# Optimization experiments

Measured on AMD Instinct MI355X. Metric: run time of the kernel, lower is better.

## Reference

```python
import jax, jax.numpy as jnp
import numpy as np

B, T, C = 2, 2048, 1024
HS, DS = 8, 32      # short heads, short qk dim
HL, DL = 8, 128     # long heads, long qk dim
HD = 64             # value/output head dim = n_embd // n_head
WIN_S, WIN_L = 256, 1024
NEG = jnp.finfo(jnp.float32).min


def _window_mask(t, window):
    # additive mask: disallow future (i<j) and tokens older than the window
    i = jnp.arange(t)[:, None]
    j = jnp.arange(t)[None, :]
    bad = (i - j < 0) | (i - j >= window)
    return bad.astype(jnp.float32) * NEG  # [T,T]


def _attn(x, Wqk, Wv, n_h, d_qk, d_v, window):
    b, t, _ = x.shape
    qk = x @ Wqk                                      # [B,T,2*n_h*d_qk]
    q, k = jnp.split(qk, 2, axis=-1)
    q = q.reshape(b, t, n_h, d_qk).transpose(0, 2, 1, 3)  # [B,H,T,dqk]
    k = k.reshape(b, t, n_h, d_qk).transpose(0, 2, 1, 3)
    v = (x @ Wv).reshape(b, t, n_h, d_v).transpose(0, 2, 1, 3)  # [B,H,T,dv]
    scale = 1.0 / jnp.sqrt(jnp.float32(d_qk))
    scores = jnp.einsum('bhqd,bhkd->bhqk', q, k) * scale
    scores = scores + _window_mask(t, window)
    p = jax.nn.softmax(scores, axis=-1)
    return jnp.einsum('bhqk,bhkd->bhqd', p, v)        # [B,H,T,dv]


def setup_inputs() -> dict:
    key = jax.random.key(0)
    ks = jax.random.split(key, 6)
    s = 0.02
    return {
        'x': jax.random.normal(ks[0], (B, T, C), dtype=jnp.float32),
        'Wqk_short': jax.random.normal(ks[1], (C, 2 * HS * DS), dtype=jnp.float32) * s,
        'Wv_short': jax.random.normal(ks[2], (C, HS * HD), dtype=jnp.float32) * s,
        'Wqk_long': jax.random.normal(ks[3], (C, 2 * HL * DL), dtype=jnp.float32) * s,
        'Wv_long': jax.random.normal(ks[4], (C, HL * HD), dtype=jnp.float32) * s,
        'Wproj': jax.random.normal(ks[5], (C, C), dtype=jnp.float32) * s,
    }


def reference(x, Wqk_short, Wv_short, Wqk_long, Wv_long, Wproj):
    b, t, c = x.shape
    y_short = _attn(x, Wqk_short, Wv_short, HS, DS, HD, WIN_S)  # [B,HS,T,HD]
    y_long = _attn(x, Wqk_long, Wv_long, HL, DL, HD, WIN_L)     # [B,HL,T,HD]
    y = jnp.concatenate([y_short, y_long], axis=1)              # [B,H,T,HD]
    y = y.transpose(0, 2, 1, 3).reshape(b, t, c)
    return y @ Wproj
```

## Files before the change

kernel.cpp:

```cpp
#include <hip/hip_runtime.h>
#include <math.h>

#define B_    2
#define T_    2048
#define C_    1024
#define HS_   8
#define DS_   32
#define HL_   8
#define DL_   128
#define HD_   64
#define WINS_ 256
#define WINL_ 1024
#define NALL_ 3584

typedef __bf16 bf16x8 __attribute__((ext_vector_type(8)));
typedef float floatx4 __attribute__((ext_vector_type(4)));

__device__ __forceinline__ ushort f2bf(float f) {
    union { float f; unsigned u; } v; v.f = f;
    unsigned r = v.u + 0x7fff + ((v.u >> 16) & 1);
    return (ushort)(r >> 16);
}

__device__ __forceinline__ void gload_lds16(const void* g, void* l) {
    __builtin_amdgcn_global_load_lds(
        (const __attribute__((address_space(1))) void*)g,
        (__attribute__((address_space(3))) void*)l, 16, 0, 0);
}

__global__ __launch_bounds__(256) void prep(
    const float* __restrict__ x, ushort* __restrict__ x16,
    const float* __restrict__ Wqk_s, const float* __restrict__ Wv_s,
    const float* __restrict__ Wqk_l, const float* __restrict__ Wv_l,
    const float* __restrict__ Wproj, ushort* __restrict__ WallT,
    ushort* __restrict__ WprojT) {
    __shared__ float t[32][33];
    int bid = blockIdx.x;
    if (bid < 4096) {
        const int i = bid * 256 + threadIdx.x;
        float4 v = ((const float4*)x)[i];
        ushort4 o;
        o.x = f2bf(v.x); o.y = f2bf(v.y); o.z = f2bf(v.z); o.w = f2bf(v.w);
        ((ushort4*)x16)[i] = o;
        return;
    }
    bid -= 4096;
    const float* W; ushort* WT; int N, rowoff;
    if (bid < 512)       { W = Wqk_s; WT = WallT;  N = 512;  rowoff = 0; }
    else if (bid < 1024) { bid -= 512;  W = Wv_s;  WT = WallT;  N = 512;  rowoff = 512; }
    else if (bid < 3072) { bid -= 1024; W = Wqk_l; WT = WallT;  N = 2048; rowoff = 1024; }
    else if (bid < 3584) { bid -= 3072; W = Wv_l;  WT = WallT;  N = 512;  rowoff = 3072; }
    else                 { bid -= 3584; W = Wproj; WT = WprojT; N = 1024; rowoff = 0; }
    const int nt = N / 32;
    const int n0 = (bid % nt) * 32;
    const int k0 = (bid / nt) * 32;
    const int tx = threadIdx.x & 31;
    const int ty = threadIdx.x >> 5;
#pragma unroll
    for (int i = 0; i < 4; ++i)
        t[ty + 8 * i][tx] = W[(size_t)(k0 + ty + 8 * i) * N + n0 + tx];
    __syncthreads();
#pragma unroll
    for (int i = 0; i < 4; ++i)
        WT[(size_t)(rowoff + n0 + ty + 8 * i) * 1024 + k0 + tx] =
            f2bf(t[tx][ty + 8 * i]);
}

template <typename OT>
__global__ __launch_bounds__(256) void gemm_bf16(const ushort* __restrict__ A,
                                                 const ushort* __restrict__ BT,
                                                 OT* __restrict__ Cm,
                                                 int M, int N, int K) {
    __shared__ ushort As[128 * 32];
    __shared__ ushort Bs[128 * 32];
    const int tid = threadIdx.x;
    const int m0 = blockIdx.y * 128;
    const int n0 = blockIdx.x * 128;
    const int wave = tid >> 6;
    const int lane = tid & 63;
    const int wm = (wave >> 1) * 64;
    const int wn = (wave & 1) * 64;
    const int l15 = lane & 15;
    const int quad = lane >> 4;

    const int srow = tid >> 2;
    const int sc = (tid & 3) * 8;

    floatx4 acc[4][4] = {};

    const ushort* Ap0 = A + (size_t)(m0 + srow) * K + sc;
    const ushort* Ap1 = A + (size_t)(m0 + srow + 64) * K + sc;
    const ushort* Bp0 = BT + (size_t)(n0 + srow) * K + sc;
    const ushort* Bp1 = BT + (size_t)(n0 + srow + 64) * K + sc;

    ushort* AsB0 = &As[wave * 512];
    ushort* AsB1 = &As[wave * 512 + 2048];
    ushort* BsB0 = &Bs[wave * 512];
    ushort* BsB1 = &Bs[wave * 512 + 2048];

    for (int kt = 0; kt < K; kt += 32) {
        __syncthreads();
        gload_lds16(Ap0 + kt, AsB0);
        gload_lds16(Ap1 + kt, AsB1);
        gload_lds16(Bp0 + kt, BsB0);
        gload_lds16(Bp1 + kt, BsB1);
        __syncthreads();

        bf16x8 af[4], bfr[4];
#pragma unroll
        for (int i = 0; i < 4; ++i)
            af[i] = *(const bf16x8*)&As[(wm + i * 16 + l15) * 32 + quad * 8];
#pragma unroll
        for (int j = 0; j < 4; ++j)
            bfr[j] = *(const bf16x8*)&Bs[(wn + j * 16 + l15) * 32 + quad * 8];
#pragma unroll
        for (int i = 0; i < 4; ++i)
#pragma unroll
            for (int j = 0; j < 4; ++j)
                acc[i][j] = __builtin_amdgcn_mfma_f32_16x16x32_bf16(
                    af[i], bfr[j], acc[i][j], 0, 0, 0);
    }

#pragma unroll
    for (int i = 0; i < 4; ++i)
#pragma unroll
        for (int j = 0; j < 4; ++j)
#pragma unroll
            for (int r = 0; r < 4; ++r) {
                const size_t idx = (size_t)(m0 + wm + i * 16 + quad * 4 + r) * N +
                                   n0 + wn + j * 16 + l15;
                if constexpr (sizeof(OT) == 2)
                    Cm[idx] = f2bf(acc[i][j][r]);
                else
                    Cm[idx] = acc[i][j][r];
            }
}

__global__ __launch_bounds__(256) void vtrans(const ushort* __restrict__ act,
                                              ushort* __restrict__ vt) {
    __shared__ ushort tile[64][72];
    const int t0 = blockIdx.x * 64;
    const int gh = blockIdx.y;
    const int b = blockIdx.z;
    const int col = (gh < 8) ? (512 + gh * 64) : (3072 + (gh - 8) * 64);
    const ushort* src = act + (size_t)(b * T_ + t0) * NALL_ + col;
    {
        const int tr = threadIdx.x >> 2;
        const int ch = threadIdx.x & 3;
        *(int4*)&tile[tr][ch * 8] =
            *(const int4*)(src + (size_t)tr * NALL_ + ch * 8);
        *(int4*)&tile[tr][(ch + 4) * 8] =
            *(const int4*)(src + (size_t)tr * NALL_ + (ch + 4) * 8);
    }
    __syncthreads();
    const int d = threadIdx.x >> 2;
    const int ts = (threadIdx.x & 3) * 16;
    ushort tmp[16];
#pragma unroll
    for (int i = 0; i < 16; ++i) tmp[i] = tile[ts + i][d];
    ushort* dst = vt + ((size_t)(b * 16 + gh) * HD_ + d) * T_ + t0 + ts;
    *(int4*)dst = *(int4*)tmp;
    *(int4*)(dst + 8) = *(int4*)(tmp + 8);
}

template <int D, int WIN, bool SPLIT>
__device__ __forceinline__ void attn_dev(
    const ushort* __restrict__ act, const ushort* __restrict__ vt,
    ushort* __restrict__ y, float* __restrict__ po, float* __restrict__ pm,
    float* __restrict__ pl, float scale, int qoff, int koff, int head_off,
    int h, int gh, int b, int t0, int zs, ushort* lds) {
    constexpr int STR = D + 8;
    constexpr int PSTR = 72;
    constexpr int NKS = D / 32;
    constexpr int QCH = D / 8;
    constexpr int NKLD = (64 * QCH) / 256;

    ushort* Ks = lds;
    ushort* VTs = Ks + 64 * STR;
    ushort* Ps = VTs + 64 * PSTR;

    const int tid = threadIdx.x;
    const int wave = tid >> 6;
    const int lane = tid & 63;
    const int l15 = lane & 15;
    const int quad = lane >> 4;
    const int qmin = t0 + wave * 16;

    int k0s = t0 - WIN + 1;
    if (k0s < 0) k0s = 0;
    k0s &= ~63;

    int ks_begin = k0s, ks_last = t0;
    if (SPLIT) {
        const int nt = ((t0 - k0s) >> 6) + 1;
        const int ntlo = (nt + 1) >> 1;
        if (zs == 0) {
            ks_last = k0s + (ntlo - 1) * 64;
        } else {
            if (ntlo >= nt) {
#pragma unroll
                for (int r = 0; r < 4; ++r) {
                    const int t = qmin + quad * 4 + r;
                    const size_t ridx =
                        (((size_t)(zs * 2 + b) * 8 + h) * T_ + t);
                    if (l15 == 0) { pm[ridx] = -1e30f; pl[ridx] = 0.f; }
#pragma unroll
                    for (int j = 0; j < 4; ++j)
                        po[ridx * 64 + j * 16 + l15] = 0.f;
                }
                return;
            }
            ks_begin = k0s + ntlo * 64;
        }
    }

    const ushort* qbase = act + (size_t)(b * T_ + t0) * NALL_ + qoff + h * D;
    const ushort* kbase = act + (size_t)(b * T_) * NALL_ + koff + h * D;
    const ushort* vtb = vt + (size_t)((b * 16 + gh) * HD_) * T_;

    int krow[NKLD], kch[NKLD];
#pragma unroll
    for (int i = 0; i < NKLD; ++i) {
        const int idx = tid + 256 * i;
        krow[i] = idx / QCH;
        kch[i] = idx % QCH;
    }
    const int vd0 = tid >> 3, vc0 = (tid & 7) * 8;
    const int vd1 = (tid + 256) >> 3, vc1 = ((tid + 256) & 7) * 8;

    int4 kreg[NKLD], vreg0, vreg1;
#pragma unroll
    for (int i = 0; i < NKLD; ++i)
        kreg[i] =
            *(const int4*)(kbase + (size_t)(ks_begin + krow[i]) * NALL_ + kch[i] * 8);
    vreg0 = *(const int4*)(vtb + (size_t)vd0 * T_ + ks_begin + vc0);
    vreg1 = *(const int4*)(vtb + (size_t)vd1 * T_ + ks_begin + vc1);

    for (int idx = tid; idx < 64 * QCH; idx += 256) {
        const int row = idx / QCH;
        const int ch = idx % QCH;
        *(int4*)&Ks[row * STR + ch * 8] =
            *(const int4*)(qbase + (size_t)row * NALL_ + ch * 8);
    }
    __syncthreads();
    bf16x8 qa[NKS];
#pragma unroll
    for (int ks = 0; ks < NKS; ++ks)
        qa[ks] = *(const bf16x8*)&Ks[(wave * 16 + l15) * STR + ks * 32 + quad * 8];

    float m_i[4], l_i[4];
    floatx4 o_acc[4] = {};
#pragma unroll
    for (int r = 0; r < 4; ++r) { m_i[r] = -1e30f; l_i[r] = 0.f; }

    for (int k0 = ks_begin; k0 <= ks_last; k0 += 64) {
        __syncthreads();
#pragma unroll
        for (int i = 0; i < NKLD; ++i)
            *(int4*)&Ks[krow[i] * STR + kch[i] * 8] = kreg[i];
        *(int4*)&VTs[vd0 * PSTR + vc0] = vreg0;
        *(int4*)&VTs[vd1 * PSTR + vc1] = vreg1;
        __syncthreads();
        if (k0 + 64 <= ks_last) {
#pragma unroll
            for (int i = 0; i < NKLD; ++i)
                kreg[i] = *(const int4*)(kbase +
                                         (size_t)(k0 + 64 + krow[i]) * NALL_ +
                                         kch[i] * 8);
            vreg0 = *(const int4*)(vtb + (size_t)vd0 * T_ + k0 + 64 + vc0);
            vreg1 = *(const int4*)(vtb + (size_t)vd1 * T_ + k0 + 64 + vc1);
        }

        floatx4 s[4] = {};
#pragma unroll
        for (int ks = 0; ks < NKS; ++ks) {
#pragma unroll
            for (int j = 0; j < 4; ++j) {
                const bf16x8 bb =
                    *(const bf16x8*)&Ks[(j * 16 + l15) * STR + ks * 32 + quad * 8];
                s[j] = __builtin_amdgcn_mfma_f32_16x16x32_bf16(qa[ks], bb, s[j],
                                                               0, 0, 0);
            }
        }

        const bool full = (k0 + 63 <= qmin) && ((qmin + 15) - k0 <= WIN - 1);
        if (full) {
#pragma unroll
            for (int j = 0; j < 4; ++j)
#pragma unroll
                for (int r = 0; r < 4; ++r) s[j][r] *= scale;
        } else {
#pragma unroll
            for (int j = 0; j < 4; ++j) {
                const int kj = k0 + j * 16 + l15;
#pragma unroll
                for (int r = 0; r < 4; ++r) {
                    const int rel = (qmin + quad * 4 + r) - kj;
                    s[j][r] = (rel < 0 || rel >= WIN) ? -1e30f : s[j][r] * scale;
                }
            }
        }

#pragma unroll
        for (int r = 0; r < 4; ++r) {
            float rm = fmaxf(fmaxf(s[0][r], s[1][r]), fmaxf(s[2][r], s[3][r]));
            rm = fmaxf(rm, __shfl_xor(rm, 1, 64));
            rm = fmaxf(rm, __shfl_xor(rm, 2, 64));
            rm = fmaxf(rm, __shfl_xor(rm, 4, 64));
            rm = fmaxf(rm, __shfl_xor(rm, 8, 64));
            const float mn = fmaxf(m_i[r], rm);
            const float a = __expf(m_i[r] - mn);
            m_i[r] = mn;
            float sum = 0.f;
#pragma unroll
            for (int j = 0; j < 4; ++j) {
                const float e = __expf(s[j][r] - mn);
                sum += e;
                Ps[(wave * 16 + quad * 4 + r) * PSTR + j * 16 + l15] = f2bf(e);
            }
            sum += __shfl_xor(sum, 1, 64);
            sum += __shfl_xor(sum, 2, 64);
            sum += __shfl_xor(sum, 4, 64);
            sum += __shfl_xor(sum, 8, 64);
            l_i[r] = l_i[r] * a + sum;
#pragma unroll
            for (int j = 0; j < 4; ++j) o_acc[j][r] *= a;
        }

#pragma unroll
        for (int kks = 0; kks < 2; ++kks) {
            const bf16x8 pa =
                *(const bf16x8*)&Ps[(wave * 16 + l15) * PSTR + kks * 32 + quad * 8];
#pragma unroll
            for (int j = 0; j < 4; ++j) {
                const bf16x8 vb =
                    *(const bf16x8*)&VTs[(j * 16 + l15) * PSTR + kks * 32 + quad * 8];
                o_acc[j] = __builtin_amdgcn_mfma_f32_16x16x32_bf16(pa, vb, o_acc[j],
                                                                   0, 0, 0);
            }
        }
    }

    if (SPLIT) {
#pragma unroll
        for (int r = 0; r < 4; ++r) {
            const int t = qmin + quad * 4 + r;
            const size_t ridx = (((size_t)(zs * 2 + b) * 8 + h) * T_ + t);
            if (l15 == 0) { pm[ridx] = m_i[r]; pl[ridx] = l_i[r]; }
#pragma unroll
            for (int j = 0; j < 4; ++j)
                po[ridx * 64 + j * 16 + l15] = o_acc[j][r];
        }
    } else {
#pragma unroll
        for (int r = 0; r < 4; ++r) {
            const float inv = 1.f / l_i[r];
            ushort* yrow = y + (size_t)(b * T_ + qmin + quad * 4 + r) * C_ +
                           head_off + h * HD_;
#pragma unroll
            for (int j = 0; j < 4; ++j)
                yrow[j * 16 + l15] = f2bf(o_acc[j][r] * inv);
        }
    }
}

__global__ __launch_bounds__(256, 4) void attn_sched(
    const ushort* __restrict__ act, const ushort* __restrict__ vt,
    ushort* __restrict__ y, float* __restrict__ po, float* __restrict__ pm,
    float* __restrict__ pl) {
    extern __shared__ ushort smem[];
    int x = blockIdx.x;
    if (x < 1024) {
        const int zs = x & 1;
        const int b = (x >> 1) & 1;
        const int h = (x >> 2) & 7;
        const int t0 = (31 - (x >> 5)) * 64;
        attn_dev<DL_, WINL_, true>(act, vt, y, po, pm, pl,
                                   0.08838834764831843f, 1024, 2048, 512, h,
                                   8 + h, b, t0, zs, smem);
    } else {
        x -= 1024;
        const int b = x & 1;
        const int h = (x >> 1) & 7;
        const int t0 = (31 - (x >> 4)) * 64;
        attn_dev<DS_, WINS_, false>(act, vt, y, po, pm, pl,
                                    0.17677669529663687f, 0, 256, 0, h, h, b,
                                    t0, 0, smem);
    }
}

__global__ __launch_bounds__(256) void combine(const float* __restrict__ po,
                                               const float* __restrict__ pm,
                                               const float* __restrict__ pl,
                                               ushort* __restrict__ y) {
    const int gid = blockIdx.x * 256 + threadIdx.x;
    const int row = gid >> 4;
    const int cg = (gid & 15) * 4;
    const int b = row >> 14;
    const int h = (row >> 11) & 7;
    const int t = row & 2047;

    const float m0 = pm[row], m1 = pm[32768 + row];
    const float l0 = pl[row], l1 = pl[32768 + row];
    const float4 o0 = *(const float4*)&po[(size_t)row * 64 + cg];
    const float4 o1 = *(const float4*)&po[(size_t)32768 * 64 + (size_t)row * 64 + cg];

    const float m = fmaxf(m0, m1);
    const float e0 = __expf(m0 - m);
    const float e1 = __expf(m1 - m);
    const float inv = 1.f / (l0 * e0 + l1 * e1);

    ushort4 r;
    r.x = f2bf((o0.x * e0 + o1.x * e1) * inv);
    r.y = f2bf((o0.y * e0 + o1.y * e1) * inv);
    r.z = f2bf((o0.z * e0 + o1.z * e1) * inv);
    r.w = f2bf((o0.w * e0 + o1.w * e1) * inv);
    *(ushort4*)&y[(size_t)(b * T_ + t) * C_ + 512 + h * 64 + cg] = r;
}

extern "C" void kernel_launch(void* const* d_in, const int* in_sizes, int n_in,
                              void* d_out, int out_size, void* d_ws,
                              size_t ws_size, hipStream_t stream) {
    const float* x         = (const float*)d_in[0];
    const float* Wqk_short = (const float*)d_in[1];
    const float* Wv_short  = (const float*)d_in[2];
    const float* Wqk_long  = (const float*)d_in[3];
    const float* Wv_long   = (const float*)d_in[4];
    const float* Wproj     = (const float*)d_in[5];
    float* out = (float*)d_out;

    const int M = B_ * T_;

    ushort* x16    = (ushort*)d_ws;
    ushort* WallT  = x16 + (size_t)M * C_;
    ushort* WprojT = WallT + (size_t)NALL_ * C_;
    ushort* yb16   = WprojT + (size_t)C_ * C_;
    ushort* act    = yb16 + (size_t)M * C_;
    ushort* vt     = act + (size_t)M * NALL_;
    float*  po     = (float*)(vt + (size_t)32 * HD_ * T_);
    float*  pm     = po + (size_t)2 * 32768 * 64;
    float*  pl     = pm + (size_t)2 * 32768;

    dim3 blk(256);
    prep<<<dim3(8704), blk, 0, stream>>>(x, x16, Wqk_short, Wv_short, Wqk_long,
                                         Wv_long, Wproj, WallT, WprojT);

    gemm_bf16<ushort><<<dim3(NALL_ / 128, M / 128), blk, 0, stream>>>(
        x16, WallT, act, M, NALL_, C_);

    vtrans<<<dim3(T_ / 64, 16, B_), blk, 0, stream>>>(act, vt);

    const int attn_lds = (64 * (DL_ + 8) + 64 * 72 * 2) * 2;
    attn_sched<<<dim3(1536), blk, attn_lds, stream>>>(act, vt, yb16, po, pm, pl);

    combine<<<dim3(2048), blk, 0, stream>>>(po, pm, pl, yb16);

    gemm_bf16<float><<<dim3(C_ / 128, M / 128), blk, 0, stream>>>(
        yb16, WprojT, out, M, C_, C_);
}
```

Baseline: 231.8 us.

## Split long-window attention four ways, store bf16 partials, use 64-row output GEMM tiles

The long-head attention KV range is now split into four partitions instead of two, giving 2048 long blocks plus the short blocks. This spreads work more evenly across CUs. Partial outputs are stored as bf16 instead of fp32 to cut the extra partial traffic, and the combine kernel now merges four partials. The projection GEMM uses 64-row M tiles so more blocks fill the GPU. Costs are more partial reads and writes, more precision loss in the partial sums, and empty partitions for short query ranges.

```diff
diff --git a/kernel.cpp b/kernel.cpp
--- a/kernel.cpp
+++ b/kernel.cpp
@@ -20,6 +20,10 @@
     union { float f; unsigned u; } v; v.f = f;
     unsigned r = v.u + 0x7fff + ((v.u >> 16) & 1);
     return (ushort)(r >> 16);
+}
+__device__ __forceinline__ float bf2f(ushort u) {
+    union { unsigned u; float f; } v; v.u = ((unsigned)u) << 16;
+    return v.f;
 }
 
 __device__ __forceinline__ void gload_lds16(const void* g, void* l) {
@@ -66,19 +70,20 @@
             f2bf(t[tx][ty + 8 * i]);
 }
 
-template <typename OT>
+template <int BM, typename OT>
 __global__ __launch_bounds__(256) void gemm_bf16(const ushort* __restrict__ A,
                                                  const ushort* __restrict__ BT,
                                                  OT* __restrict__ Cm,
                                                  int M, int N, int K) {
-    __shared__ ushort As[128 * 32];
+    __shared__ ushort As[BM * 32];
     __shared__ ushort Bs[128 * 32];
+    constexpr int NI = BM / 32;
     const int tid = threadIdx.x;
-    const int m0 = blockIdx.y * 128;
+    const int m0 = blockIdx.y * BM;
     const int n0 = blockIdx.x * 128;
     const int wave = tid >> 6;
     const int lane = tid & 63;
-    const int wm = (wave >> 1) * 64;
+    const int wm = (wave >> 1) * (BM / 2);
     const int wn = (wave & 1) * 64;
     const int l15 = lane & 15;
     const int quad = lane >> 4;
@@ -86,35 +91,35 @@
     const int srow = tid >> 2;
     const int sc = (tid & 3) * 8;
 
-    floatx4 acc[4][4] = {};
+    floatx4 acc[NI][4] = {};
 
     const ushort* Ap0 = A + (size_t)(m0 + srow) * K + sc;
-    const ushort* Ap1 = A + (size_t)(m0 + srow + 64) * K + sc;
+    const ushort* Ap1 = A + (size_t)(m0 + (srow & 63) + 64) * K + sc;
     const ushort* Bp0 = BT + (size_t)(n0 + srow) * K + sc;
     const ushort* Bp1 = BT + (size_t)(n0 + srow + 64) * K + sc;
 
     ushort* AsB0 = &As[wave * 512];
-    ushort* AsB1 = &As[wave * 512 + 2048];
+    ushort* AsB1 = &As[(wave * 512 + 2048) % (BM * 32)];
     ushort* BsB0 = &Bs[wave * 512];
     ushort* BsB1 = &Bs[wave * 512 + 2048];
 
     for (int kt = 0; kt < K; kt += 32) {
         __syncthreads();
         gload_lds16(Ap0 + kt, AsB0);
-        gload_lds16(Ap1 + kt, AsB1);
+        if constexpr (BM == 128) gload_lds16(Ap1 + kt, AsB1);
         gload_lds16(Bp0 + kt, BsB0);
         gload_lds16(Bp1 + kt, BsB1);
         __syncthreads();
 
-        bf16x8 af[4], bfr[4];
-#pragma unroll
-        for (int i = 0; i < 4; ++i)
+        bf16x8 af[NI], bfr[4];
+#pragma unroll
+        for (int i = 0; i < NI; ++i)
             af[i] = *(const bf16x8*)&As[(wm + i * 16 + l15) * 32 + quad * 8];
 #pragma unroll
         for (int j = 0; j < 4; ++j)
             bfr[j] = *(const bf16x8*)&Bs[(wn + j * 16 + l15) * 32 + quad * 8];
 #pragma unroll
-        for (int i = 0; i < 4; ++i)
+        for (int i = 0; i < NI; ++i)
 #pragma unroll
             for (int j = 0; j < 4; ++j)
                 acc[i][j] = __builtin_amdgcn_mfma_f32_16x16x32_bf16(
@@ -122,7 +127,7 @@
     }
 
 #pragma unroll
-    for (int i = 0; i < 4; ++i)
+    for (int i = 0; i < NI; ++i)
 #pragma unroll
         for (int j = 0; j < 4; ++j)
 #pragma unroll
@@ -166,7 +171,7 @@
 template <int D, int WIN, bool SPLIT>
 __device__ __forceinline__ void attn_dev(
     const ushort* __restrict__ act, const ushort* __restrict__ vt,
-    ushort* __restrict__ y, float* __restrict__ po, float* __restrict__ pm,
+    ushort* __restrict__ y, ushort* __restrict__ po, float* __restrict__ pm,
     float* __restrict__ pl, float scale, int qoff, int koff, int head_off,
     int h, int gh, int b, int t0, int zs, ushort* lds) {
     constexpr int STR = D + 8;
@@ -193,25 +198,21 @@
     int ks_begin = k0s, ks_last = t0;
     if (SPLIT) {
         const int nt = ((t0 - k0s) >> 6) + 1;
-        const int ntlo = (nt + 1) >> 1;
-        if (zs == 0) {
-            ks_last = k0s + (ntlo - 1) * 64;
-        } else {
-            if (ntlo >= nt) {
-#pragma unroll
-                for (int r = 0; r < 4; ++r) {
-                    const int t = qmin + quad * 4 + r;
-                    const size_t ridx =
-                        (((size_t)(zs * 2 + b) * 8 + h) * T_ + t);
-                    if (l15 == 0) { pm[ridx] = -1e30f; pl[ridx] = 0.f; }
-#pragma unroll
-                    for (int j = 0; j < 4; ++j)
-                        po[ridx * 64 + j * 16 + l15] = 0.f;
-                }
-                return;
-            }
-            ks_begin = k0s + ntlo * 64;
-        }
+        const int tb = (zs * nt) >> 2;
+        const int te = ((zs + 1) * nt) >> 2;
+        if (tb >= te) {
+#pragma unroll
+            for (int r = 0; r < 4; ++r) {
+                const int t = qmin + quad * 4 + r;
+                const size_t ridx = (((size_t)(zs * 2 + b) * 8 + h) * T_ + t);
+                if (l15 == 0) { pm[ridx] = -1e30f; pl[ridx] = 0.f; }
+#pragma unroll
+                for (int j = 0; j < 4; ++j) po[ridx * 64 + j * 16 + l15] = 0;
+            }
+            return;
+        }
+        ks_begin = k0s + tb * 64;
+        ks_last = k0s + (te - 1) * 64;
     }
 
     const ushort* qbase = act + (size_t)(b * T_ + t0) * NALL_ + qoff + h * D;
@@ -231,8 +232,8 @@
     int4 kreg[NKLD], vreg0, vreg1;
 #pragma unroll
     for (int i = 0; i < NKLD; ++i)
-        kreg[i] =
-            *(const int4*)(kbase + (size_t)(ks_begin + krow[i]) * NALL_ + kch[i] * 8);
+        kreg[i] = *(const int4*)(kbase + (size_t)(ks_begin + krow[i]) * NALL_ +
+                                 kch[i] * 8);
     vreg0 = *(const int4*)(vtb + (size_t)vd0 * T_ + ks_begin + vc0);
     vreg1 = *(const int4*)(vtb + (size_t)vd1 * T_ + ks_begin + vc1);
 
@@ -349,7 +350,7 @@
             if (l15 == 0) { pm[ridx] = m_i[r]; pl[ridx] = l_i[r]; }
 #pragma unroll
             for (int j = 0; j < 4; ++j)
-                po[ridx * 64 + j * 16 + l15] = o_acc[j][r];
+                po[ridx * 64 + j * 16 + l15] = f2bf(o_acc[j][r]);
         }
     } else {
 #pragma unroll
@@ -366,20 +367,20 @@
 
 __global__ __launch_bounds__(256, 4) void attn_sched(
     const ushort* __restrict__ act, const ushort* __restrict__ vt,
-    ushort* __restrict__ y, float* __restrict__ po, float* __restrict__ pm,
+    ushort* __restrict__ y, ushort* __restrict__ po, float* __restrict__ pm,
     float* __restrict__ pl) {
     extern __shared__ ushort smem[];
     int x = blockIdx.x;
-    if (x < 1024) {
-        const int zs = x & 1;
-        const int b = (x >> 1) & 1;
-        const int h = (x >> 2) & 7;
-        const int t0 = (31 - (x >> 5)) * 64;
+    if (x < 2048) {
+        const int zs = x & 3;
+        const int b = (x >> 2) & 1;
+        const int h = (x >> 3) & 7;
+        const int t0 = (31 - (x >> 6)) * 64;
         attn_dev<DL_, WINL_, true>(act, vt, y, po, pm, pl,
                                    0.08838834764831843f, 1024, 2048, 512, h,
                                    8 + h, b, t0, zs, smem);
     } else {
-        x -= 1024;
+        x -= 2048;
         const int b = x & 1;
         const int h = (x >> 1) & 7;
         const int t0 = (31 - (x >> 4)) * 64;
@@ -389,7 +390,7 @@
     }
 }
 
-__global__ __launch_bounds__(256) void combine(const float* __restrict__ po,
+__global__ __launch_bounds__(256) void combine(const ushort* __restrict__ po,
                                                const float* __restrict__ pm,
                                                const float* __restrict__ pl,
                                                ushort* __restrict__ y) {
@@ -400,21 +401,28 @@
     const int h = (row >> 11) & 7;
     const int t = row & 2047;
 
-    const float m0 = pm[row], m1 = pm[32768 + row];
-    const float l0 = pl[row], l1 = pl[32768 + row];
-    const float4 o0 = *(const float4*)&po[(size_t)row * 64 + cg];
-    const float4 o1 = *(const float4*)&po[(size_t)32768 * 64 + (size_t)row * 64 + cg];
-
-    const float m = fmaxf(m0, m1);
-    const float e0 = __expf(m0 - m);
-    const float e1 = __expf(m1 - m);
-    const float inv = 1.f / (l0 * e0 + l1 * e1);
-
+    float m = -1e30f;
+#pragma unroll
+    for (int s = 0; s < 4; ++s) m = fmaxf(m, pm[s * 32768 + row]);
+    float l = 0.f;
+    float acc[4] = {};
+#pragma unroll
+    for (int s = 0; s < 4; ++s) {
+        const float e = __expf(pm[s * 32768 + row] - m);
+        l += pl[s * 32768 + row] * e;
+        const ushort4 o =
+            *(const ushort4*)&po[((size_t)s * 32768 + row) * 64 + cg];
+        acc[0] += bf2f(o.x) * e;
+        acc[1] += bf2f(o.y) * e;
+        acc[2] += bf2f(o.z) * e;
+        acc[3] += bf2f(o.w) * e;
+    }
+    const float inv = 1.f / l;
     ushort4 r;
-    r.x = f2bf((o0.x * e0 + o1.x * e1) * inv);
-    r.y = f2bf((o0.y * e0 + o1.y * e1) * inv);
-    r.z = f2bf((o0.z * e0 + o1.z * e1) * inv);
-    r.w = f2bf((o0.w * e0 + o1.w * e1) * inv);
+    r.x = f2bf(acc[0] * inv);
+    r.y = f2bf(acc[1] * inv);
+    r.z = f2bf(acc[2] * inv);
+    r.w = f2bf(acc[3] * inv);
     *(ushort4*)&y[(size_t)(b * T_ + t) * C_ + 512 + h * 64 + cg] = r;
 }
 
@@ -437,24 +445,24 @@
     ushort* yb16   = WprojT + (size_t)C_ * C_;
     ushort* act    = yb16 + (size_t)M * C_;
     ushort* vt     = act + (size_t)M * NALL_;
-    float*  po     = (float*)(vt + (size_t)32 * HD_ * T_);
-    float*  pm     = po + (size_t)2 * 32768 * 64;
-    float*  pl     = pm + (size_t)2 * 32768;
+    ushort* po     = vt + (size_t)32 * HD_ * T_;
+    float*  pm     = (float*)(po + (size_t)4 * 32768 * 64);
+    float*  pl     = pm + (size_t)4 * 32768;
 
     dim3 blk(256);
     prep<<<dim3(8704), blk, 0, stream>>>(x, x16, Wqk_short, Wv_short, Wqk_long,
                                          Wv_long, Wproj, WallT, WprojT);
 
-    gemm_bf16<ushort><<<dim3(NALL_ / 128, M / 128), blk, 0, stream>>>(
+    gemm_bf16<128, ushort><<<dim3(NALL_ / 128, M / 128), blk, 0, stream>>>(
         x16, WallT, act, M, NALL_, C_);
 
     vtrans<<<dim3(T_ / 64, 16, B_), blk, 0, stream>>>(act, vt);
 
     const int attn_lds = (64 * (DL_ + 8) + 64 * 72 * 2) * 2;
-    attn_sched<<<dim3(1536), blk, attn_lds, stream>>>(act, vt, yb16, po, pm, pl);
+    attn_sched<<<dim3(2560), blk, attn_lds, stream>>>(act, vt, yb16, po, pm, pl);
 
     combine<<<dim3(2048), blk, 0, stream>>>(po, pm, pl, yb16);
 
-    gemm_bf16<float><<<dim3(C_ / 128, M / 128), blk, 0, stream>>>(
+    gemm_bf16<64, float><<<dim3(C_ / 128, M / 64), blk, 0, stream>>>(
         yb16, WprojT, out, M, C_, C_);
 }
```

Result: slower. 242.1 us (+4.5%).
